# Optimization experiments

Hardware: AMD Instinct MI355X
Metric: run time of the kernel (lower is better)

## Reference

```python
import jax, jax.numpy as jnp
import numpy as np
from jax import lax

H = 8          # num_heads
STATE = 16     # SSM state_dim
EPS = 1e-5


def layer_norm(x, g, b):
    mu = jnp.mean(x, axis=-1, keepdims=True)
    var = jnp.mean((x - mu) ** 2, axis=-1, keepdims=True)
    return (x - mu) / jnp.sqrt(var + EPS) * g + b


def linear(x, w, b):
    # torch nn.Linear convention: w [out,in]
    return x @ w.T + b


def cross_attn(q_in, kv_in, qw, qb, kw, kb, vw, vb, ow, ob, g, beta):
    B, Lq, D = q_in.shape
    Lk = kv_in.shape[1]
    hd = D // H
    Q = linear(q_in, qw, qb).reshape(B, Lq, H, hd).transpose(0, 2, 1, 3)
    K = linear(kv_in, kw, kb).reshape(B, Lk, H, hd).transpose(0, 2, 1, 3)
    V = linear(kv_in, vw, vb).reshape(B, Lk, H, hd).transpose(0, 2, 1, 3)
    scores = jnp.einsum('bhqd,bhkd->bhqk', Q, K) / (hd ** 0.5)
    w = jax.nn.softmax(scores, axis=-1)
    out = jnp.einsum('bhqk,bhkd->bhqd', w, V)
    out = out.transpose(0, 2, 1, 3).reshape(B, Lq, D)
    out = linear(out, ow, ob)
    out = layer_norm(out + q_in, g, beta)
    return out, w


def ssm(x, in_w, in_b, A, Bm, C, gw, gb, ow, ob):
    B, L, D = x.shape
    xp = linear(x, in_w, in_b)                      # [B,L,2D]
    x_in = xp[..., D:]                              # second chunk
    gate = jax.nn.sigmoid(linear(x, gw, gb))
    x_in = x_in * gate
    def step(h, xt):
        h = h @ A.T + xt @ Bm.T                     # [B,STATE]
        return h, h @ C.T                           # y [B,D]
    h0 = jnp.zeros((B, STATE), dtype=x.dtype)
    _, ys = lax.scan(step, h0, x_in.transpose(1, 0, 2))
    ys = ys.transpose(1, 0, 2)
    return linear(ys, ow, ob)


def mamba_block(x, p, i):
    y = ssm(layer_norm(x, p['m_ln1_g'][i], p['m_ln1_b'][i]),
            p['m_in_w'][i], p['m_in_b'][i], p['m_A'][i], p['m_B'][i], p['m_C'][i],
            p['m_gate_w'][i], p['m_gate_b'][i], p['m_sout_w'][i], p['m_sout_b'][i])
    x = x + y
    h = layer_norm(x, p['m_ln2_g'][i], p['m_ln2_b'][i])
    h = linear(h, p['m_f1_w'][i], p['m_f1_b'][i])
    h = jax.nn.gelu(h, approximate=False)
    h = linear(h, p['m_f2_w'][i], p['m_f2_b'][i])
    return x + h


def setup_inputs() -> dict:
    key = jax.random.key(0)
    ks = iter(jax.random.split(key, 64))
    B, L, D, BD, VD = 1024, 32, 256, 128, 256
    nB = 6
    def rn(shape, s=0.02):
        return jax.random.normal(next(ks), shape, dtype=jnp.float32) * s
    inp = {
        'ble_features': jax.random.normal(next(ks), (B, L, BD), dtype=jnp.float32),
        'visual_features': jax.random.normal(next(ks), (B, L, VD), dtype=jnp.float32),
        # modality projections
        'bp_w': rn((D, BD)), 'bp_b': jnp.zeros(D), 'bp_emb': rn((D,)),
        'bp_g': jnp.ones(D), 'bp_beta': jnp.zeros(D),
        'vp_w': rn((D, VD)), 'vp_b': jnp.zeros(D), 'vp_emb': rn((D,)),
        'vp_g': jnp.ones(D), 'vp_beta': jnp.zeros(D),
        # two cross-attentions stacked on axis 0: [0]=ble->vis, [1]=vis->ble
        'a_qw': rn((2, D, D)), 'a_qb': jnp.zeros((2, D)),
        'a_kw': rn((2, D, D)), 'a_kb': jnp.zeros((2, D)),
        'a_vw': rn((2, D, D)), 'a_vb': jnp.zeros((2, D)),
        'a_ow': rn((2, D, D)), 'a_ob': jnp.zeros((2, D)),
        'a_g': jnp.ones((2, D)), 'a_beta': jnp.zeros((2, D)),
        # 6 mamba blocks stacked on axis 0
        'm_ln1_g': jnp.ones((nB, D)), 'm_ln1_b': jnp.zeros((nB, D)),
        'm_in_w': rn((nB, 2 * D, D)), 'm_in_b': jnp.zeros((nB, 2 * D)),
        'm_A': rn((nB, STATE, STATE)), 'm_B': rn((nB, STATE, D)), 'm_C': rn((nB, D, STATE)),
        'm_gate_w': rn((nB, D, D)), 'm_gate_b': jnp.zeros((nB, D)),
        'm_sout_w': rn((nB, D, D)), 'm_sout_b': jnp.zeros((nB, D)),
        'm_ln2_g': jnp.ones((nB, D)), 'm_ln2_b': jnp.zeros((nB, D)),
        'm_f1_w': rn((nB, 4 * D, D)), 'm_f1_b': jnp.zeros((nB, 4 * D)),
        'm_f2_w': rn((nB, D, 4 * D)), 'm_f2_b': jnp.zeros((nB, D)),
        # final projection
        'fin_g': jnp.ones(D), 'fin_beta': jnp.zeros(D),
        'fin_w': rn((D, D)), 'fin_b': jnp.zeros(D),
    }
    return inp


def reference(ble_features, visual_features,
              bp_w, bp_b, bp_emb, bp_g, bp_beta,
              vp_w, vp_b, vp_emb, vp_g, vp_beta,
              a_qw, a_qb, a_kw, a_kb, a_vw, a_vb, a_ow, a_ob, a_g, a_beta,
              m_ln1_g, m_ln1_b, m_in_w, m_in_b, m_A, m_B, m_C,
              m_gate_w, m_gate_b, m_sout_w, m_sout_b,
              m_ln2_g, m_ln2_b, m_f1_w, m_f1_b, m_f2_w, m_f2_b,
              fin_g, fin_beta, fin_w, fin_b):
    ble = layer_norm(linear(ble_features, bp_w, bp_b) + bp_emb, bp_g, bp_beta)
    vis = layer_norm(linear(visual_features, vp_w, vp_b) + vp_emb, vp_g, vp_beta)
    # seq_len == target_length -> align_sequences is identity
    ble_att, w_b2v = cross_attn(ble, vis, a_qw[0], a_qb[0], a_kw[0], a_kb[0],
                                a_vw[0], a_vb[0], a_ow[0], a_ob[0], a_g[0], a_beta[0])
    vis_att, w_v2b = cross_attn(vis, ble, a_qw[1], a_qb[1], a_kw[1], a_kb[1],
                                a_vw[1], a_vb[1], a_ow[1], a_ob[1], a_g[1], a_beta[1])
    fused = ble_att + vis_att
    p = dict(m_ln1_g=m_ln1_g, m_ln1_b=m_ln1_b, m_in_w=m_in_w, m_in_b=m_in_b,
             m_A=m_A, m_B=m_B, m_C=m_C, m_gate_w=m_gate_w, m_gate_b=m_gate_b,
             m_sout_w=m_sout_w, m_sout_b=m_sout_b, m_ln2_g=m_ln2_g, m_ln2_b=m_ln2_b,
             m_f1_w=m_f1_w, m_f1_b=m_f1_b, m_f2_w=m_f2_w, m_f2_b=m_f2_b)
    for i in range(m_A.shape[0]):
        fused = mamba_block(fused, p, i)
    g = jnp.mean(fused, axis=1)
    g = layer_norm(g, fin_g, fin_beta)
    g = jax.nn.gelu(linear(g, fin_w, fin_b), approximate=False)
    wb = jnp.mean(w_b2v, axis=(1, 2, 3))
    wv = jnp.mean(w_v2b, axis=(1, 2, 3))
    tot = wb + wv + 1e-6
    return (g, wb / tot, wv / tot)
```

## Files before the change

### kernel.cpp

```cpp
#include <hip/hip_runtime.h>
#include <hip/hip_bf16.h>
#include <math.h>

static constexpr int Bsz  = 1024;
static constexpr int Lseq = 32;
static constexpr int Dm   = 256;
static constexpr int NROW = Bsz * Lseq;

typedef __attribute__((ext_vector_type(8))) short bf16x8;
typedef __attribute__((ext_vector_type(4))) float f32x4;

__device__ __forceinline__ float sigm_f(float x) {
    return 1.0f / (1.0f + __expf(-x));
}
__device__ __forceinline__ float gelu_f(float x) {
    const float u = x * (0.7978845608028654f + 0.0356774081f * x * x);
    return x * sigm_f(2.0f * u);
}
__device__ __forceinline__ float b2f(ushort u) {
    union { float f; uint v; } t; t.v = ((uint)u) << 16; return t.f;
}
__device__ __forceinline__ ushort f2b(float f) {
    union { float f; uint v; } t; t.f = f;
    const uint lsb = (t.v >> 16) & 1u;
    t.v += 0x7fffu + lsb;
    return (ushort)(t.v >> 16);
}

#define GLDS(gp, lp) __builtin_amdgcn_global_load_lds( \
    (const __attribute__((address_space(1))) void*)(gp), \
    (__attribute__((address_space(3))) void*)(lp), 16, 0, 0)

template<int ACT, bool OUTBF, int OMAP, int DUAL>
__global__ __launch_bounds__(256)
void mgemm(const ushort* __restrict__ X, const ushort* __restrict__ W,
           const ushort* __restrict__ W2,
           const float* __restrict__ b1, const float* __restrict__ b2,
           float* __restrict__ Cf, ushort* __restrict__ Cb,
           ushort* __restrict__ Cb2, int K, int M)
{
    __shared__ ushort As[4096];
    __shared__ ushort Bs[4096];
    __shared__ ushort Bs2[DUAL ? 4096 : 8];
    __shared__ ushort Rx[DUAL ? 4096 : 8192];
    const int tid = threadIdx.x;
    const int w = tid >> 6, l = tid & 63;

    int f = blockIdx.y * gridDim.x + blockIdx.x;
    const int nwg = gridDim.x * gridDim.y;
    if ((nwg & 7) == 0) f = (f & 7) * (nwg >> 3) + (f >> 3);
    const int n0 = (f / gridDim.x) << 7;
    const int m0 = (f % gridDim.x) << 7;

    const int ric  = l >> 2;
    const int slot = l & 3;
    const int rL0 = (w << 4) + ric;
    const int rL1 = rL0 + 64;
    const int sw0 = slot ^ ((rL0 >> 1) & 3);
    const int sw1 = slot ^ ((rL1 >> 1) & 3);
    const ushort* gA0 = X + (size_t)(n0 + rL0) * K + (sw0 << 3);
    const ushort* gA1 = X + (size_t)(n0 + rL1) * K + (sw1 << 3);
    const ushort* gB0 = W + (size_t)(m0 + rL0) * K + (sw0 << 3);
    const ushort* gB1 = W + (size_t)(m0 + rL1) * K + (sw1 << 3);
    const ushort* gC0 = nullptr; const ushort* gC1 = nullptr;
    if constexpr (DUAL) {
        gC0 = W2 + (size_t)(m0 + rL0) * K + (sw0 << 3);
        gC1 = W2 + (size_t)(m0 + rL1) * K + (sw1 << 3);
    }
    ushort* lA0 = As + ((size_t)w << 9);
    ushort* lA1 = As + ((size_t)(w + 4) << 9);
    ushort* lB0 = Bs + ((size_t)w << 9);
    ushort* lB1 = Bs + ((size_t)(w + 4) << 9);
    ushort* lC0 = Bs2 + ((size_t)w << 9);
    ushort* lC1 = Bs2 + ((size_t)(w + 4) << 9);

    const int wr = (w >> 1) & 1, wc = w & 1;
    const int cl = l & 15, kg = l >> 4;
    int aoff[4], boff[4];
    #pragma unroll
    for (int m = 0; m < 4; ++m) {
        const int r = wr * 64 + m * 16 + cl;
        aoff[m] = r * 32 + ((kg ^ ((r >> 1) & 3)) << 3);
    }
    #pragma unroll
    for (int n = 0; n < 4; ++n) {
        const int r = wc * 64 + n * 16 + cl;
        boff[n] = r * 32 + ((kg ^ ((r >> 1) & 3)) << 3);
    }

    f32x4 acc[4][4];
    f32x4 acc2[DUAL ? 4 : 1][DUAL ? 4 : 1];
    #pragma unroll
    for (int m = 0; m < 4; ++m)
        #pragma unroll
        for (int n = 0; n < 4; ++n) {
            acc[m][n] = (f32x4){0.f, 0.f, 0.f, 0.f};
            if constexpr (DUAL) acc2[m][n] = (f32x4){0.f, 0.f, 0.f, 0.f};
        }

    for (int kc = 0; kc < K; kc += 32) {
        GLDS(gA0, lA0); GLDS(gA1, lA1);
        GLDS(gB0, lB0); GLDS(gB1, lB1);
        gA0 += 32; gA1 += 32; gB0 += 32; gB1 += 32;
        if constexpr (DUAL) {
            GLDS(gC0, lC0); GLDS(gC1, lC1);
            gC0 += 32; gC1 += 32;
        }
        __syncthreads();
        bf16x8 av[4], bv[4];
        #pragma unroll
        for (int m = 0; m < 4; ++m) av[m] = *(const bf16x8*)(As + aoff[m]);
        #pragma unroll
        for (int n = 0; n < 4; ++n) bv[n] = *(const bf16x8*)(Bs + boff[n]);
        #pragma unroll
        for (int m = 0; m < 4; ++m)
            #pragma unroll
            for (int n = 0; n < 4; ++n)
                acc[m][n] = __builtin_amdgcn_mfma_f32_16x16x32_bf16(
                    av[m], bv[n], acc[m][n], 0, 0, 0);
        if constexpr (DUAL) {
            bf16x8 cv[4];
            #pragma unroll
            for (int n = 0; n < 4; ++n) cv[n] = *(const bf16x8*)(Bs2 + boff[n]);
            #pragma unroll
            for (int m = 0; m < 4; ++m)
                #pragma unroll
                for (int n = 0; n < 4; ++n)
                    acc2[m][n] = __builtin_amdgcn_mfma_f32_16x16x32_bf16(
                        av[m], cv[n], acc2[m][n], 0, 0, 0);
        }
        __syncthreads();
    }

    const int colb = m0 + wc * 64 + cl;
    const int rowb = n0 + wr * 64 + (kg << 2);
    float biasA[4], biasB[4];
    #pragma unroll
    for (int n = 0; n < 4; ++n) {
        biasA[n] = (b1 != nullptr) ? b1[colb + n * 16] : 0.0f;
        if constexpr (DUAL) biasB[n] = b2[colb + n * 16];
    }

    if constexpr (OUTBF || DUAL != 0) {
        ushort* Rw;
        if constexpr (DUAL) Rw = (w == 0) ? As : (w == 1) ? Bs : (w == 2) ? Bs2 : Rx;
        else                Rw = (w == 0) ? As : (w == 1) ? Bs : Rx + ((w - 2) << 12);
        const int rr = l >> 3, rc8 = (l & 7) << 3;
        const int nout = (DUAL == 2) ? 2 : 1;
        for (int which = 0; which < nout; ++which) {
            #pragma unroll
            for (int m = 0; m < 4; ++m)
                #pragma unroll
                for (int j = 0; j < 4; ++j) {
                    const int lrow = m * 16 + (kg << 2) + j;
                    #pragma unroll
                    for (int n = 0; n < 4; ++n) {
                        float v;
                        if (which == 0) {
                            v = acc[m][n][j] + biasA[n];
                            if constexpr (DUAL == 1)
                                v = sigm_f(v) * (acc2[m][n][j] + biasB[n]);
                            else if (ACT == 1) v = sigm_f(v);
                            else if (ACT == 2) v = gelu_f(v);
                        } else {
                            v = acc2[m][n][j] + biasB[n];
                        }
                        const int lcol = (n << 4) + cl;
                        Rw[lrow * 64 + (lcol ^ (((lrow >> 1) & 7) << 3))] = f2b(v);
                    }
                }
            ushort* dst = (which == 0) ? Cb : Cb2;
            #pragma unroll
            for (int p = 0; p < 8; ++p) {
                const int lrow = (p << 3) + rr;
                const bf16x8 v8 = *(const bf16x8*)(
                    Rw + lrow * 64 + (rc8 ^ (((lrow >> 1) & 7) << 3)));
                const size_t grow = (size_t)(n0 + wr * 64 + lrow);
                const int gcol = m0 + wc * 64 + rc8;
                size_t idx;
                if (OMAP == 1) idx = grow * 1024 + ((size_t)(gcol >> 4) << 5) + (gcol & 15);
                else           idx = grow * (size_t)M + gcol;
                *(bf16x8*)(dst + idx) = v8;
            }
        }
    } else {
        #pragma unroll
        for (int m = 0; m < 4; ++m)
            #pragma unroll
            for (int j = 0; j < 4; ++j) {
                const size_t row = (size_t)(rowb + m * 16 + j);
                #pragma unroll
                for (int n = 0; n < 4; ++n) {
                    float v = acc[m][n][j] + biasA[n];
                    if (ACT == 1) v = sigm_f(v);
                    else if (ACT == 2) v = gelu_f(v);
                    Cf[row * (size_t)M + colb + n * 16] = v;
                }
            }
    }
}

template<bool ADD_E, bool ACC_F, bool WRV, int LNOUT, bool HASB2>
__global__ __launch_bounds__(256)
void growln_k(const ushort* __restrict__ X, const ushort* __restrict__ W,
              const float* __restrict__ b1, const float* __restrict__ b2,
              const float* __restrict__ E, const float* __restrict__ g,
              const float* __restrict__ bt, float* __restrict__ Fres,
              ushort* __restrict__ Yb, int K)
{
    __shared__ ushort As[32 * 32];
    __shared__ ushort Bs[256 * 32];
    __shared__ float sred[32][2];
    __shared__ float qred[32][2];
    const int tid = threadIdx.x;
    const int w = tid >> 6, l = tid & 63;
    const int n0 = blockIdx.x << 5;
    const int rowg = w >> 1, colg = w & 1;

    const int ric = l >> 2, slot = l & 3;
    const ushort* gB[4]; ushort* lB[4];
    #pragma unroll
    for (int c = 0; c < 4; ++c) {
        const int rB = ((w << 2) + c) * 16 + ric;
        gB[c] = W + (size_t)rB * K + ((slot ^ ((rB >> 1) & 3)) << 3);
        lB[c] = Bs + (((w << 2) + c) << 9);
    }
    const ushort* gA = nullptr; ushort* lA = nullptr;
    if (w < 2) {
        const int rA = (w << 4) + ric;
        gA = X + (size_t)(n0 + rA) * K + ((slot ^ ((rA >> 1) & 3)) << 3);
        lA = As + (w << 9);
    }

    const int cl = l & 15, kg = l >> 4;
    const int ar = rowg * 16 + cl;
    const int aoff = ar * 32 + ((kg ^ ((ar >> 1) & 3)) << 3);
    int boff[8];
    #pragma unroll
    for (int n = 0; n < 8; ++n) {
        const int br = colg * 128 + n * 16 + cl;
        boff[n] = br * 32 + ((kg ^ ((br >> 1) & 3)) << 3);
    }

    f32x4 acc[8];
    #pragma unroll
    for (int n = 0; n < 8; ++n) acc[n] = (f32x4){0.f, 0.f, 0.f, 0.f};

    for (int kc = 0; kc < K; kc += 32) {
        #pragma unroll
        for (int c = 0; c < 4; ++c) { GLDS(gB[c], lB[c]); gB[c] += 32; }
        if (w < 2) { GLDS(gA, lA); gA += 32; }
        __syncthreads();
        const bf16x8 av = *(const bf16x8*)(As + aoff);
        #pragma unroll
        for (int n = 0; n < 8; ++n) {
            const bf16x8 bv = *(const bf16x8*)(Bs + boff[n]);
            acc[n] = __builtin_amdgcn_mfma_f32_16x16x32_bf16(av, bv, acc[n], 0, 0, 0);
        }
        __syncthreads();
    }

    float bA[8];
    #pragma unroll
    for (int n = 0; n < 8; ++n) {
        const int col = colg * 128 + n * 16 + cl;
        float v = (b1 != nullptr) ? b1[col] : 0.0f;
        if (HASB2) v += b2[col];
        bA[n] = v;
    }
    float gg[8], bb[8];
    if (LNOUT > 0) {
        #pragma unroll
        for (int n = 0; n < 8; ++n) {
            const int col = colg * 128 + n * 16 + cl;
            gg[n] = g[col]; bb[n] = bt[col];
        }
    }

    #pragma unroll
    for (int j = 0; j < 4; ++j) {
        const int lrow = rowg * 16 + (kg << 2) + j;
        const size_t rb = (size_t)(n0 + lrow) << 8;
        float s = 0.0f;
        #pragma unroll
        for (int n = 0; n < 8; ++n) {
            const size_t idx = rb + colg * 128 + n * 16 + cl;
            float x = acc[n][j] + bA[n];
            if (ADD_E) x += E[idx];
            if (ACC_F) x += Fres[idx];
            acc[n][j] = x; s += x;
        }
        if (WRV) {
            #pragma unroll
            for (int n = 0; n < 8; ++n)
                Fres[rb + colg * 128 + n * 16 + cl] = acc[n][j];
        }
        if (LNOUT > 0) {
            #pragma unroll
            for (int o = 1; o < 16; o <<= 1) s += __shfl_xor(s, o);
            if (cl == 0) sred[lrow][colg] = s;
        }
    }
    if (LNOUT > 0) {
        __syncthreads();
        float mu[4];
        #pragma unroll
        for (int j = 0; j < 4; ++j) {
            const int lrow = rowg * 16 + (kg << 2) + j;
            mu[j] = (sred[lrow][0] + sred[lrow][1]) * (1.0f / 256.0f);
            float q = 0.0f;
            #pragma unroll
            for (int n = 0; n < 8; ++n) { const float d = acc[n][j] - mu[j]; q += d * d; }
            #pragma unroll
            for (int o = 1; o < 16; o <<= 1) q += __shfl_xor(q, o);
            if (cl == 0) qred[lrow][colg] = q;
        }
        __syncthreads();
        #pragma unroll
        for (int j = 0; j < 4; ++j) {
            const int lrow = rowg * 16 + (kg << 2) + j;
            const size_t rb = (size_t)(n0 + lrow) << 8;
            const float rstd = rsqrtf((qred[lrow][0] + qred[lrow][1]) * (1.0f / 256.0f) + 1e-5f);
            #pragma unroll
            for (int n = 0; n < 8; ++n) {
                const float y = (acc[n][j] - mu[j]) * rstd * gg[n] + bb[n];
                const size_t idx = rb + colg * 128 + n * 16 + cl;
                if (LNOUT & 1) Yb[idx] = f2b(y);
                if (LNOUT == 2 || LNOUT == 3) Fres[idx] = y;
                if (LNOUT == 4) Fres[idx] += y;
            }
        }
    }
}

__global__ __launch_bounds__(256)
void ln_k(const float* __restrict__ X, const float* __restrict__ g,
          const float* __restrict__ bt, ushort* __restrict__ Yb)
{
    const int lane = threadIdx.x & 63;
    const int row  = (blockIdx.x << 2) + (threadIdx.x >> 6);
    const size_t base = (size_t)row * Dm + (lane << 2);
    float4 v = *reinterpret_cast<const float4*>(&X[base]);
    float s = v.x + v.y + v.z + v.w;
    #pragma unroll
    for (int o = 1; o < 64; o <<= 1) s += __shfl_xor(s, o);
    const float mu = s * (1.0f / 256.0f);
    const float d0 = v.x - mu, d1 = v.y - mu, d2 = v.z - mu, d3 = v.w - mu;
    float q = d0*d0 + d1*d1 + d2*d2 + d3*d3;
    #pragma unroll
    for (int o = 1; o < 64; o <<= 1) q += __shfl_xor(q, o);
    const float rstd = rsqrtf(q * (1.0f / 256.0f) + 1e-5f);
    const int c = lane << 2;
    const float4 gg = *reinterpret_cast<const float4*>(&g[c]);
    const float4 bb = *reinterpret_cast<const float4*>(&bt[c]);
    ushort4 ub;
    ub.x = f2b(d0*rstd*gg.x + bb.x); ub.y = f2b(d1*rstd*gg.y + bb.y);
    ub.z = f2b(d2*rstd*gg.z + bb.z); ub.w = f2b(d3*rstd*gg.w + bb.w);
    *reinterpret_cast<ushort4*>(&Yb[base]) = ub;
}

__global__ __launch_bounds__(256)
void attn_k(const ushort* __restrict__ Q, const ushort* __restrict__ K,
            const ushort* __restrict__ V, ushort* __restrict__ O)
{
    __shared__ float Qs[32][33], Ks[32][33], Vs[32][33], Ss[32][33];
    const int bh = blockIdx.x;
    const int b = bh >> 3, h = bh & 7;
    const int tid = threadIdx.x;
    const int r  = tid >> 3;
    const int c4 = (tid & 7) << 2;
    const size_t base = ((size_t)b * Lseq + r) * Dm + h * 32 + c4;
    {
        const ushort4 q = *reinterpret_cast<const ushort4*>(&Q[base]);
        Qs[r][c4+0]=b2f(q.x); Qs[r][c4+1]=b2f(q.y); Qs[r][c4+2]=b2f(q.z); Qs[r][c4+3]=b2f(q.w);
        const ushort4 k = *reinterpret_cast<const ushort4*>(&K[base]);
        Ks[r][c4+0]=b2f(k.x); Ks[r][c4+1]=b2f(k.y); Ks[r][c4+2]=b2f(k.z); Ks[r][c4+3]=b2f(k.w);
        const ushort4 v = *reinterpret_cast<const ushort4*>(&V[base]);
        Vs[r][c4+0]=b2f(v.x); Vs[r][c4+1]=b2f(v.y); Vs[r][c4+2]=b2f(v.z); Vs[r][c4+3]=b2f(v.w);
    }
    __syncthreads();
    float sc[4] = {0.f, 0.f, 0.f, 0.f};
    #pragma unroll
    for (int d = 0; d < 32; ++d) {
        const float qv = Qs[r][d];
        #pragma unroll
        for (int j = 0; j < 4; ++j) sc[j] = fmaf(qv, Ks[c4+j][d], sc[j]);
    }
    #pragma unroll
    for (int j = 0; j < 4; ++j) sc[j] *= 0.17677669529663687f;
    float mx = fmaxf(fmaxf(sc[0], sc[1]), fmaxf(sc[2], sc[3]));
    #pragma unroll
    for (int o = 1; o < 8; o <<= 1) mx = fmaxf(mx, __shfl_xor(mx, o));
    float sum = 0.f;
    #pragma unroll
    for (int j = 0; j < 4; ++j) { sc[j] = __expf(sc[j] - mx); sum += sc[j]; }
    #pragma unroll
    for (int o = 1; o < 8; o <<= 1) sum += __shfl_xor(sum, o);
    const float inv = 1.0f / sum;
    #pragma unroll
    for (int j = 0; j < 4; ++j) Ss[r][c4+j] = sc[j] * inv;
    __syncthreads();
    float o4[4] = {0.f, 0.f, 0.f, 0.f};
    #pragma unroll
    for (int k = 0; k < 32; ++k) {
        const float wv = Ss[r][k];
        #pragma unroll
        for (int j = 0; j < 4; ++j) o4[j] = fmaf(wv, Vs[k][c4+j], o4[j]);
    }
    ushort4 ob; ob.x=f2b(o4[0]); ob.y=f2b(o4[1]); ob.z=f2b(o4[2]); ob.w=f2b(o4[3]);
    *reinterpret_cast<ushort4*>(&O[base]) = ob;
}

__global__ __launch_bounds__(256)
void xb_gemm(const ushort* __restrict__ X, const ushort* __restrict__ Bw,
             ushort* __restrict__ XB)
{
    __shared__ ushort As[128 * 32];
    __shared__ ushort Bsf[16 * 256];
    const int tid = threadIdx.x;
    const int w = tid >> 6, l = tid & 63;
    const int n0 = blockIdx.x << 7;
    #pragma unroll
    for (int rep = 0; rep < 2; ++rep) {
        const int u = (rep << 8) + tid;
        const int r = u >> 5;
        const int c8 = (u & 31) << 3;
        const int di = (r * 256 + c8) ^ ((r & 7) << 3);
        *(bf16x8*)(Bsf + di) = *(const bf16x8*)(Bw + r * 256 + c8);
    }
    const int ric = l >> 2, slot = l & 3;
    const int rL0 = (w << 4) + ric, rL1 = rL0 + 64;
    const int sw0 = slot ^ ((rL0 >> 1) & 3), sw1 = slot ^ ((rL1 >> 1) & 3);
    const ushort* gA0 = X + (size_t)(n0 + rL0) * 256 + (sw0 << 3);
    const ushort* gA1 = X + (size_t)(n0 + rL1) * 256 + (sw1 << 3);
    ushort* lA0 = As + (w << 9);
    ushort* lA1 = As + ((w + 4) << 9);
    const int cl = l & 15, kg = l >> 4;
    int aoff[2];
    #pragma unroll
    for (int m = 0; m < 2; ++m) {
        const int r = w * 32 + m * 16 + cl;
        aoff[m] = r * 32 + ((kg ^ ((r >> 1) & 3)) << 3);
    }
    f32x4 acc[2] = {(f32x4){0.f,0.f,0.f,0.f}, (f32x4){0.f,0.f,0.f,0.f}};
    for (int kc = 0; kc < 256; kc += 32) {
        GLDS(gA0, lA0); GLDS(gA1, lA1);
        gA0 += 32; gA1 += 32;
        __syncthreads();
        const bf16x8 av0 = *(const bf16x8*)(As + aoff[0]);
        const bf16x8 av1 = *(const bf16x8*)(As + aoff[1]);
        const int bidx = (cl * 256 + kc + (kg << 3)) ^ ((cl & 7) << 3);
        const bf16x8 bv = *(const bf16x8*)(Bsf + bidx);
        acc[0] = __builtin_amdgcn_mfma_f32_16x16x32_bf16(av0, bv, acc[0], 0, 0, 0);
        acc[1] = __builtin_amdgcn_mfma_f32_16x16x32_bf16(av1, bv, acc[1], 0, 0, 0);
        __syncthreads();
    }
    #pragma unroll
    for (int m = 0; m < 2; ++m)
        #pragma unroll
        for (int j = 0; j < 4; ++j) {
            const int row = n0 + w * 32 + m * 16 + (kg << 2) + j;
            XB[(size_t)row * 16 + cl] = f2b(acc[m][j]);
        }
}

__global__ __launch_bounds__(256)
void powT_k(const float* __restrict__ A_all, ushort* __restrict__ T_all)
{
    __shared__ float P[2][16][16];
    __shared__ float Asm[16][16];
    const int layer = blockIdx.x;
    const float* A = A_all + layer * 256;
    ushort* T = T_all + (size_t)layer * 262144;
    const int tid = threadIdx.x;
    const int i = tid >> 4, j = tid & 15;
    Asm[i][j] = A[tid];
    const bf16x8 z = {0,0,0,0,0,0,0,0};
    for (int u = tid; u < 32768; u += 256)
        *(bf16x8*)(T + (size_t)u * 8) = z;
    P[0][i][j] = (i == j) ? 1.0f : 0.0f;
    __syncthreads();
    for (int k = 0; k < 32; ++k) {
        const float pv = P[k & 1][i][j];
        const ushort pb = f2b(pv);
        for (int tau = 0; tau + k < 32; ++tau)
            T[(size_t)((tau + k) * 16 + i) * 512 + tau * 16 + j] = pb;
        float acc = 0.0f;
        #pragma unroll
        for (int l2 = 0; l2 < 16; ++l2) acc = fmaf(P[k & 1][i][l2], Asm[l2][j], acc);
        P[(k & 1) ^ 1][i][j] = acc;
        __syncthreads();
    }
}

__global__ __launch_bounds__(256)
void zeroH_k(ushort* __restrict__ Hp)
{
    const int i = blockIdx.x * 256 + threadIdx.x;
    const bf16x8 z = {0,0,0,0,0,0,0,0};
    *(bf16x8*)(Hp + (size_t)i * 8) = z;
}

__global__ __launch_bounds__(256)
void wsc_k(const float* __restrict__ sw, const float* __restrict__ Cc,
           ushort* __restrict__ Wp)
{
    const int i = blockIdx.x >> 4;
    const int m = ((blockIdx.x & 15) << 4) + (threadIdx.x >> 4);
    const int s = threadIdx.x & 15;
    const float* swr = sw + ((size_t)i << 16) + (m << 8);
    const float* cc  = Cc + ((size_t)i << 12) + s;
    float acc = 0.0f;
    #pragma unroll 8
    for (int d = 0; d < 256; ++d) acc = fmaf(swr[d], cc[d << 4], acc);
    ushort* o = Wp + ((size_t)i << 13) + (m << 5);
    o[s] = f2b(acc);
    o[s + 16] = 0;
}

__global__ __launch_bounds__(256)
void meanL_k(const float* __restrict__ X, float* __restrict__ G)
{
    const int idx = blockIdx.x * 256 + threadIdx.x;
    const int b = idx >> 8, d = idx & 255;
    const float* xp = X + (size_t)b * (Lseq * Dm) + d;
    float s = 0.0f;
    #pragma unroll
    for (int t = 0; t < Lseq; ++t) s += xp[t << 8];
    G[idx] = s * (1.0f / 32.0f);
}

__global__ __launch_bounds__(256)
void fillw_k(float* __restrict__ out)
{
    const int i = blockIdx.x * 256 + threadIdx.x;
    const float wm = 1.0f / 32.0f;
    out[i] = wm / (wm + wm + 1e-6f);
}

__global__ __launch_bounds__(256)
void cast_k(const float* __restrict__ src, ushort* __restrict__ dst, int n4)
{
    const int i = blockIdx.x * 256 + threadIdx.x;
    if (i < n4) {
        const float4 v = reinterpret_cast<const float4*>(src)[i];
        ushort4 o; o.x = f2b(v.x); o.y = f2b(v.y); o.z = f2b(v.z); o.w = f2b(v.w);
        reinterpret_cast<ushort4*>(dst)[i] = o;
    }
}

__global__ __launch_bounds__(256)
void cast_inw_k(const float* __restrict__ src, ushort* __restrict__ dst)
{
    const int i = blockIdx.x * 256 + threadIdx.x;
    const int blk = i >> 14, rem = i & 16383;
    const float4 v = reinterpret_cast<const float4*>(
        src + (size_t)blk * 131072 + 65536)[rem];
    ushort4 o; o.x = f2b(v.x); o.y = f2b(v.y); o.z = f2b(v.z); o.w = f2b(v.w);
    reinterpret_cast<ushort4*>(dst)[i] = o;
}

extern "C" void kernel_launch(void* const* d_in, const int* in_sizes, int n_in,
                              void* d_out, int out_size, void* d_ws, size_t ws_size,
                              hipStream_t stream)
{
    const float* ble_f   = (const float*)d_in[0];
    const float* vis_f   = (const float*)d_in[1];
    const float* bp_w    = (const float*)d_in[2];
    const float* bp_b    = (const float*)d_in[3];
    const float* bp_emb  = (const float*)d_in[4];
    const float* bp_g    = (const float*)d_in[5];
    const float* bp_beta = (const float*)d_in[6];
    const float* vp_w    = (const float*)d_in[7];
    const float* vp_b    = (const float*)d_in[8];
    const float* vp_emb  = (const float*)d_in[9];
    const float* vp_g    = (const float*)d_in[10];
    const float* vp_beta = (const float*)d_in[11];
    const float* a_qw    = (const float*)d_in[12];
    const float* a_qb    = (const float*)d_in[13];
    const float* a_kw    = (const float*)d_in[14];
    const float* a_kb    = (const float*)d_in[15];
    const float* a_vw    = (const float*)d_in[16];
    const float* a_vb    = (const float*)d_in[17];
    const float* a_ow    = (const float*)d_in[18];
    const float* a_ob    = (const float*)d_in[19];
    const float* a_g     = (const float*)d_in[20];
    const float* a_beta  = (const float*)d_in[21];
    const float* m_ln1_g = (const float*)d_in[22];
    const float* m_ln1_b = (const float*)d_in[23];
    const float* m_in_w  = (const float*)d_in[24];
    const float* m_in_b  = (const float*)d_in[25];
    const float* m_A     = (const float*)d_in[26];
    const float* m_B     = (const float*)d_in[27];
    const float* m_C     = (const float*)d_in[28];
    const float* m_gw    = (const float*)d_in[29];
    const float* m_gb    = (const float*)d_in[30];
    const float* m_sw    = (const float*)d_in[31];
    const float* m_sb    = (const float*)d_in[32];
    const float* m_ln2_g = (const float*)d_in[33];
    const float* m_ln2_b = (const float*)d_in[34];
    const float* m_f1w   = (const float*)d_in[35];
    const float* m_f1b   = (const float*)d_in[36];
    const float* m_f2w   = (const float*)d_in[37];
    const float* m_f2b   = (const float*)d_in[38];
    const float* fin_g   = (const float*)d_in[39];
    const float* fin_beta= (const float*)d_in[40];
    const float* fin_w   = (const float*)d_in[41];
    const float* fin_b   = (const float*)d_in[42];

    float* out = (float*)d_out;
    float* ws  = (float*)d_ws;
    const size_t NDf = (size_t)NROW * Dm;

    float* F_res = ws;
    float* F0 = ws + 1 * NDf;
    float* F1 = ws + 2 * NDf;
    float* F2 = ws + 3 * NDf;
    ushort* S0 = (ushort*)(ws + 4 * NDf);
    ushort* S1 = S0 + NDf;
    ushort* S2 = S1 + NDf;
    ushort* S3 = S2 + NDf;
    ushort* S4 = S3 + NDf;
    ushort* Wa = S4 + NDf;
    ushort* W_bp  = Wa;
    ushort* W_vp  = W_bp + 32768;
    ushort* W_q   = W_vp + 65536;
    ushort* W_k   = W_q + 131072;
    ushort* W_v   = W_k + 131072;
    ushort* W_o   = W_v + 131072;
    ushort* W_g   = W_o + 131072;
    ushort* W_in  = W_g + 393216;
    ushort* W_f1  = W_in + 393216;
    ushort* W_f2  = W_f1 + 1572864;
    ushort* W_fin = W_f2 + 1572864;
    ushort* W_sc  = W_fin + 65536;
    ushort* Hpad  = W_sc + 49152;
    ushort* B_ble = (ushort*)F2;
    ushort* B_vis = B_ble + (size_t)NROW * 128;
    ushort* T_all = (ushort*)F2;
    ushort* W_bm  = T_all + 1572864;
    ushort* XBuf  = W_bm + 24576;

    const dim3 blk(256);
    auto cgrid = [](int n4) { return dim3((n4 + 255) / 256); };

    cast_k<<<cgrid(1048576), blk, 0, stream>>>(ble_f, B_ble, 1048576);
    cast_k<<<cgrid(2097152), blk, 0, stream>>>(vis_f, B_vis, 2097152);
    cast_k<<<cgrid(8192),   blk, 0, stream>>>(bp_w, W_bp, 8192);
    cast_k<<<cgrid(16384),  blk, 0, stream>>>(vp_w, W_vp, 16384);
    cast_k<<<cgrid(32768),  blk, 0, stream>>>(a_qw, W_q, 32768);
    cast_k<<<cgrid(32768),  blk, 0, stream>>>(a_kw, W_k, 32768);
    cast_k<<<cgrid(32768),  blk, 0, stream>>>(a_vw, W_v, 32768);
    cast_k<<<cgrid(32768),  blk, 0, stream>>>(a_ow, W_o, 32768);
    cast_k<<<cgrid(98304),  blk, 0, stream>>>(m_gw, W_g, 98304);
    cast_k<<<cgrid(393216), blk, 0, stream>>>(m_f1w, W_f1, 393216);
    cast_k<<<cgrid(393216), blk, 0, stream>>>(m_f2w, W_f2, 393216);
    cast_k<<<cgrid(16384),  blk, 0, stream>>>(fin_w, W_fin, 16384);
    cast_inw_k<<<cgrid(98304), blk, 0, stream>>>(m_in_w, W_in);
    wsc_k<<<96, blk, 0, stream>>>(m_sw, m_C, W_sc);

    auto gg = [](int M, int N) { return dim3(M / 128, N / 128); };
    const dim3 gRow(NROW / 32);

    growln_k<false,false,false,3,true><<<gRow, blk, 0, stream>>>(
        B_ble, W_bp, bp_b, bp_emb, nullptr, bp_g, bp_beta, F0, S0, 128);
    growln_k<false,false,false,3,true><<<gRow, blk, 0, stream>>>(
        B_vis, W_vp, vp_b, vp_emb, nullptr, vp_g, vp_beta, F1, S1, 256);

    for (int a = 0; a < 2; ++a) {
        const ushort* qin_b = (a == 0) ? S0 : S1;
        const ushort* kin_b = (a == 0) ? S1 : S0;
        const float*  qin_f = (a == 0) ? F0 : F1;
        const size_t wo = (size_t)a * 65536;
        const size_t bo = (size_t)a * 256;
        mgemm<0,true,0,0><<<gg(256, NROW), blk, 0, stream>>>(
            qin_b, W_q + wo, nullptr, a_qb + bo, nullptr, nullptr, S4, nullptr, 256, 256);
        mgemm<0,true,0,2><<<gg(256, NROW), blk, 0, stream>>>(
            kin_b, W_k + wo, W_v + wo, a_kb + bo, a_vb + bo, nullptr, S2, S3, 256, 256);
        attn_k<<<Bsz * 8, blk, 0, stream>>>(S4, S2, S3, S4);
        if (a == 0)
            growln_k<true,false,false,2,false><<<gRow, blk, 0, stream>>>(
                S4, W_o + wo, a_ob + bo, nullptr, qin_f, a_g + bo, a_beta + bo, F_res, nullptr, 256);
        else
            growln_k<true,false,false,4,false><<<gRow, blk, 0, stream>>>(
                S4, W_o + wo, a_ob + bo, nullptr, qin_f, a_g + bo, a_beta + bo, F_res, nullptr, 256);
    }

    powT_k<<<6, blk, 0, stream>>>(m_A, T_all);
    cast_k<<<cgrid(6144), blk, 0, stream>>>(m_B, W_bm, 6144);
    zeroH_k<<<512, blk, 0, stream>>>(Hpad);

    ln_k<<<NROW/4, blk, 0, stream>>>(F_res, m_ln1_g, m_ln1_b, S0);

    for (int i = 0; i < 6; ++i) {
        mgemm<0,true,0,1><<<gg(256, NROW), blk, 0, stream>>>(
            S0, W_g + (size_t)i*65536, W_in + (size_t)i*65536,
            m_gb + i*256, m_in_b + (size_t)i*512 + 256, nullptr, S2, nullptr, 256, 256);
        xb_gemm<<<NROW/128, blk, 0, stream>>>(S2, W_bm + (size_t)i*4096, XBuf);
        mgemm<0,true,1,0><<<gg(512, 1024), blk, 0, stream>>>(
            XBuf, T_all + (size_t)i*262144, nullptr, nullptr, nullptr, nullptr, Hpad, nullptr, 512, 512);
        growln_k<false,true,true,1,false><<<gRow, blk, 0, stream>>>(
            Hpad, W_sc + (size_t)i*8192, m_sb + i*256, nullptr, nullptr,
            m_ln2_g + i*256, m_ln2_b + i*256, F_res, S0, 32);
        mgemm<2,true,0,0><<<gg(1024, NROW), blk, 0, stream>>>(
            S0, W_f1 + (size_t)i*262144, nullptr, m_f1b + i*1024, nullptr, nullptr, S1, nullptr, 256, 1024);
        if (i < 5)
            growln_k<false,true,true,1,false><<<gRow, blk, 0, stream>>>(
                S1, W_f2 + (size_t)i*262144, m_f2b + i*256, nullptr, nullptr,
                m_ln1_g + (i+1)*256, m_ln1_b + (i+1)*256, F_res, S0, 1024);
        else
            growln_k<false,true,true,0,false><<<gRow, blk, 0, stream>>>(
                S1, W_f2 + (size_t)i*262144, m_f2b + i*256, nullptr, nullptr,
                nullptr, nullptr, F_res, nullptr, 1024);
    }

    meanL_k<<<(Bsz * Dm) / 256, blk, 0, stream>>>(F_res, F0);
    ln_k<<<Bsz/4, blk, 0, stream>>>(F0, fin_g, fin_beta, S1);
    mgemm<2,false,0,0><<<gg(256, Bsz), blk, 0, stream>>>(
        S1, W_fin, nullptr, fin_b, nullptr, out, nullptr, nullptr, 256, 256);
    fillw_k<<<8, blk, 0, stream>>>(out + (size_t)Bsz * Dm);
}
```

Measured before the change: 1.293 ms.

## Double GEMM K-tile depth to 64 in mgemm and growln kernels

Raises the per-iteration K chunk from 32 to 64 in both the generic tiled GEMM and the row GEMM+layernorm kernel, halving the number of barrier-separated load/compute iterations. LDS tiles grow and use a new 8-way XOR swizzle. Because K must now be a multiple of 64, the padded state buffer (Hpad) and the folded SSM output weights are re-laid out with 64-wide padding, doubling the padded work for the K=32 SSM projection. Larger LDS use may lower occupancy.

```diff
diff --git a/kernel.cpp b/kernel.cpp
--- a/kernel.cpp
+++ b/kernel.cpp
@@ -31,6 +31,7 @@
     (const __attribute__((address_space(1))) void*)(gp), \
     (__attribute__((address_space(3))) void*)(lp), 16, 0, 0)
 
+
 template<int ACT, bool OUTBF, int OMAP, int DUAL>
 __global__ __launch_bounds__(256)
 void mgemm(const ushort* __restrict__ X, const ushort* __restrict__ W,
@@ -39,10 +40,9 @@
            float* __restrict__ Cf, ushort* __restrict__ Cb,
            ushort* __restrict__ Cb2, int K, int M)
 {
-    __shared__ ushort As[4096];
-    __shared__ ushort Bs[4096];
-    __shared__ ushort Bs2[DUAL ? 4096 : 8];
-    __shared__ ushort Rx[DUAL ? 4096 : 8192];
+    __shared__ ushort As[8192];
+    __shared__ ushort Bs[8192];
+    __shared__ ushort Bs2[DUAL ? 8192 : 8];
     const int tid = threadIdx.x;
     const int w = tid >> 6, l = tid & 63;
 
@@ -52,40 +52,40 @@
     const int n0 = (f / gridDim.x) << 7;
     const int m0 = (f % gridDim.x) << 7;
 
-    const int ric  = l >> 2;
-    const int slot = l & 3;
-    const int rL0 = (w << 4) + ric;
-    const int rL1 = rL0 + 64;
-    const int sw0 = slot ^ ((rL0 >> 1) & 3);
-    const int sw1 = slot ^ ((rL1 >> 1) & 3);
-    const ushort* gA0 = X + (size_t)(n0 + rL0) * K + (sw0 << 3);
-    const ushort* gA1 = X + (size_t)(n0 + rL1) * K + (sw1 << 3);
-    const ushort* gB0 = W + (size_t)(m0 + rL0) * K + (sw0 << 3);
-    const ushort* gB1 = W + (size_t)(m0 + rL1) * K + (sw1 << 3);
-    const ushort* gC0 = nullptr; const ushort* gC1 = nullptr;
-    if constexpr (DUAL) {
-        gC0 = W2 + (size_t)(m0 + rL0) * K + (sw0 << 3);
-        gC1 = W2 + (size_t)(m0 + rL1) * K + (sw1 << 3);
-    }
-    ushort* lA0 = As + ((size_t)w << 9);
-    ushort* lA1 = As + ((size_t)(w + 4) << 9);
-    ushort* lB0 = Bs + ((size_t)w << 9);
-    ushort* lB1 = Bs + ((size_t)(w + 4) << 9);
-    ushort* lC0 = Bs2 + ((size_t)w << 9);
-    ushort* lC1 = Bs2 + ((size_t)(w + 4) << 9);
+    const int ric = l >> 3;
+    const int sl  = l & 7;
+    const ushort* gAp[4]; const ushort* gBp[4]; const ushort* gCp[DUAL ? 4 : 1];
+    ushort* lAp[4]; ushort* lBp[4]; ushort* lCp[DUAL ? 4 : 1];
+    #pragma unroll
+    for (int c = 0; c < 4; ++c) {
+        const int r = ((w << 2) + c) * 8 + ric;
+        const int eo = (sl ^ (r & 7)) << 3;
+        gAp[c] = X + (size_t)(n0 + r) * K + eo;
+        gBp[c] = W + (size_t)(m0 + r) * K + eo;
+        lAp[c] = As + (((w << 2) + c) << 9) ;
+        lBp[c] = Bs + (((w << 2) + c) << 9);
+        if constexpr (DUAL) {
+            gCp[c] = W2 + (size_t)(m0 + r) * K + eo;
+            lCp[c] = Bs2 + (((w << 2) + c) << 9);
+        }
+    }
 
     const int wr = (w >> 1) & 1, wc = w & 1;
     const int cl = l & 15, kg = l >> 4;
-    int aoff[4], boff[4];
-    #pragma unroll
-    for (int m = 0; m < 4; ++m) {
-        const int r = wr * 64 + m * 16 + cl;
-        aoff[m] = r * 32 + ((kg ^ ((r >> 1) & 3)) << 3);
-    }
-    #pragma unroll
-    for (int n = 0; n < 4; ++n) {
-        const int r = wc * 64 + n * 16 + cl;
-        boff[n] = r * 32 + ((kg ^ ((r >> 1) & 3)) << 3);
+    int aoff[2][4], boff[2][4];
+    #pragma unroll
+    for (int sub = 0; sub < 2; ++sub) {
+        const int s = sub * 4 + kg;
+        #pragma unroll
+        for (int m = 0; m < 4; ++m) {
+            const int r = wr * 64 + m * 16 + cl;
+            aoff[sub][m] = r * 64 + ((s ^ (r & 7)) << 3);
+        }
+        #pragma unroll
+        for (int n = 0; n < 4; ++n) {
+            const int r = wc * 64 + n * 16 + cl;
+            boff[sub][n] = r * 64 + ((s ^ (r & 7)) << 3);
+        }
     }
 
     f32x4 acc[4][4];
@@ -98,36 +98,38 @@
             if constexpr (DUAL) acc2[m][n] = (f32x4){0.f, 0.f, 0.f, 0.f};
         }
 
-    for (int kc = 0; kc < K; kc += 32) {
-        GLDS(gA0, lA0); GLDS(gA1, lA1);
-        GLDS(gB0, lB0); GLDS(gB1, lB1);
-        gA0 += 32; gA1 += 32; gB0 += 32; gB1 += 32;
-        if constexpr (DUAL) {
-            GLDS(gC0, lC0); GLDS(gC1, lC1);
-            gC0 += 32; gC1 += 32;
-        }
-        __syncthreads();
-        bf16x8 av[4], bv[4];
-        #pragma unroll
-        for (int m = 0; m < 4; ++m) av[m] = *(const bf16x8*)(As + aoff[m]);
-        #pragma unroll
-        for (int n = 0; n < 4; ++n) bv[n] = *(const bf16x8*)(Bs + boff[n]);
-        #pragma unroll
-        for (int m = 0; m < 4; ++m)
-            #pragma unroll
-            for (int n = 0; n < 4; ++n)
-                acc[m][n] = __builtin_amdgcn_mfma_f32_16x16x32_bf16(
-                    av[m], bv[n], acc[m][n], 0, 0, 0);
-        if constexpr (DUAL) {
-            bf16x8 cv[4];
-            #pragma unroll
-            for (int n = 0; n < 4; ++n) cv[n] = *(const bf16x8*)(Bs2 + boff[n]);
+    for (int kc = 0; kc < K; kc += 64) {
+        #pragma unroll
+        for (int c = 0; c < 4; ++c) {
+            GLDS(gAp[c], lAp[c]); gAp[c] += 64;
+            GLDS(gBp[c], lBp[c]); gBp[c] += 64;
+            if constexpr (DUAL) { GLDS(gCp[c], lCp[c]); gCp[c] += 64; }
+        }
+        __syncthreads();
+        #pragma unroll
+        for (int sub = 0; sub < 2; ++sub) {
+            bf16x8 av[4], bv[4];
+            #pragma unroll
+            for (int m = 0; m < 4; ++m) av[m] = *(const bf16x8*)(As + aoff[sub][m]);
+            #pragma unroll
+            for (int n = 0; n < 4; ++n) bv[n] = *(const bf16x8*)(Bs + boff[sub][n]);
             #pragma unroll
             for (int m = 0; m < 4; ++m)
                 #pragma unroll
                 for (int n = 0; n < 4; ++n)
-                    acc2[m][n] = __builtin_amdgcn_mfma_f32_16x16x32_bf16(
-                        av[m], cv[n], acc2[m][n], 0, 0, 0);
+                    acc[m][n] = __builtin_amdgcn_mfma_f32_16x16x32_bf16(
+                        av[m], bv[n], acc[m][n], 0, 0, 0);
+            if constexpr (DUAL) {
+                bf16x8 cv[4];
+                #pragma unroll
+                for (int n = 0; n < 4; ++n) cv[n] = *(const bf16x8*)(Bs2 + boff[sub][n]);
+                #pragma unroll
+                for (int m = 0; m < 4; ++m)
+                    #pragma unroll
+                    for (int n = 0; n < 4; ++n)
+                        acc2[m][n] = __builtin_amdgcn_mfma_f32_16x16x32_bf16(
+                            av[m], cv[n], acc2[m][n], 0, 0, 0);
+            }
         }
         __syncthreads();
     }
@@ -142,9 +144,8 @@
     }
 
     if constexpr (OUTBF || DUAL != 0) {
-        ushort* Rw;
-        if constexpr (DUAL) Rw = (w == 0) ? As : (w == 1) ? Bs : (w == 2) ? Bs2 : Rx;
-        else                Rw = (w == 0) ? As : (w == 1) ? Bs : Rx + ((w - 2) << 12);
+        ushort* Rw = (w == 0) ? As : (w == 1) ? As + 4096
+                   : (w == 2) ? Bs : Bs + 4096;
         const int rr = l >> 3, rc8 = (l & 7) << 3;
         const int nout = (DUAL == 2) ? 2 : 1;
         for (int which = 0; which < nout; ++which) {
@@ -178,7 +179,7 @@
                 const size_t grow = (size_t)(n0 + wr * 64 + lrow);
                 const int gcol = m0 + wc * 64 + rc8;
                 size_t idx;
-                if (OMAP == 1) idx = grow * 1024 + ((size_t)(gcol >> 4) << 5) + (gcol & 15);
+                if (OMAP == 1) idx = grow * 2048 + ((size_t)(gcol >> 4) << 6) + (gcol & 15);
                 else           idx = grow * (size_t)M + gcol;
                 *(bf16x8*)(dst + idx) = v8;
             }
@@ -208,8 +209,8 @@
               const float* __restrict__ bt, float* __restrict__ Fres,
               ushort* __restrict__ Yb, int K)
 {
-    __shared__ ushort As[32 * 32];
-    __shared__ ushort Bs[256 * 32];
+    __shared__ ushort As[32 * 64];
+    __shared__ ushort Bs[256 * 64];
     __shared__ float sred[32][2];
     __shared__ float qred[32][2];
     const int tid = threadIdx.x;
@@ -217,45 +218,49 @@
     const int n0 = blockIdx.x << 5;
     const int rowg = w >> 1, colg = w & 1;
 
-    const int ric = l >> 2, slot = l & 3;
-    const ushort* gB[4]; ushort* lB[4];
-    #pragma unroll
-    for (int c = 0; c < 4; ++c) {
-        const int rB = ((w << 2) + c) * 16 + ric;
-        gB[c] = W + (size_t)rB * K + ((slot ^ ((rB >> 1) & 3)) << 3);
-        lB[c] = Bs + (((w << 2) + c) << 9);
-    }
-    const ushort* gA = nullptr; ushort* lA = nullptr;
-    if (w < 2) {
-        const int rA = (w << 4) + ric;
-        gA = X + (size_t)(n0 + rA) * K + ((slot ^ ((rA >> 1) & 3)) << 3);
-        lA = As + (w << 9);
-    }
+    const int ric = l >> 3, sl = l & 7;
+    const ushort* gB[8]; ushort* lB[8];
+    #pragma unroll
+    for (int c = 0; c < 8; ++c) {
+        const int rB = ((w << 3) + c) * 8 + ric;
+        gB[c] = W + (size_t)rB * K + ((sl ^ (rB & 7)) << 3);
+        lB[c] = Bs + (((w << 3) + c) << 9);
+    }
+    const int rA = (w << 3) + ric;
+    const ushort* gA = X + (size_t)(n0 + rA) * K + ((sl ^ (rA & 7)) << 3);
+    ushort* lA = As + (w << 9);
 
     const int cl = l & 15, kg = l >> 4;
     const int ar = rowg * 16 + cl;
-    const int aoff = ar * 32 + ((kg ^ ((ar >> 1) & 3)) << 3);
-    int boff[8];
-    #pragma unroll
-    for (int n = 0; n < 8; ++n) {
-        const int br = colg * 128 + n * 16 + cl;
-        boff[n] = br * 32 + ((kg ^ ((br >> 1) & 3)) << 3);
+    int aoff[2], boff[2][8];
+    #pragma unroll
+    for (int sub = 0; sub < 2; ++sub) {
+        const int s = sub * 4 + kg;
+        aoff[sub] = ar * 64 + ((s ^ (ar & 7)) << 3);
+        #pragma unroll
+        for (int n = 0; n < 8; ++n) {
+            const int br = colg * 128 + n * 16 + cl;
+            boff[sub][n] = br * 64 + ((s ^ (br & 7)) << 3);
+        }
     }
 
     f32x4 acc[8];
     #pragma unroll
     for (int n = 0; n < 8; ++n) acc[n] = (f32x4){0.f, 0.f, 0.f, 0.f};
 
-    for (int kc = 0; kc < K; kc += 32) {
-        #pragma unroll
-        for (int c = 0; c < 4; ++c) { GLDS(gB[c], lB[c]); gB[c] += 32; }
-        if (w < 2) { GLDS(gA, lA); gA += 32; }
-        __syncthreads();
-        const bf16x8 av = *(const bf16x8*)(As + aoff);
-        #pragma unroll
-        for (int n = 0; n < 8; ++n) {
-            const bf16x8 bv = *(const bf16x8*)(Bs + boff[n]);
-            acc[n] = __builtin_amdgcn_mfma_f32_16x16x32_bf16(av, bv, acc[n], 0, 0, 0);
+    for (int kc = 0; kc < K; kc += 64) {
+        #pragma unroll
+        for (int c = 0; c < 8; ++c) { GLDS(gB[c], lB[c]); gB[c] += 64; }
+        GLDS(gA, lA); gA += 64;
+        __syncthreads();
+        #pragma unroll
+        for (int sub = 0; sub < 2; ++sub) {
+            const bf16x8 av = *(const bf16x8*)(As + aoff[sub]);
+            #pragma unroll
+            for (int n = 0; n < 8; ++n) {
+                const bf16x8 bv = *(const bf16x8*)(Bs + boff[sub][n]);
+                acc[n] = __builtin_amdgcn_mfma_f32_16x16x32_bf16(av, bv, acc[n], 0, 0, 0);
+            }
         }
         __syncthreads();
     }
@@ -513,9 +518,9 @@
     float acc = 0.0f;
     #pragma unroll 8
     for (int d = 0; d < 256; ++d) acc = fmaf(swr[d], cc[d << 4], acc);
-    ushort* o = Wp + ((size_t)i << 13) + (m << 5);
+    ushort* o = Wp + ((size_t)i << 14) + (m << 6);
     o[s] = f2b(acc);
-    o[s + 16] = 0;
+    o[s + 16] = 0; o[s + 32] = 0; o[s + 48] = 0;
 }
 
 __global__ __launch_bounds__(256)
@@ -634,7 +639,7 @@
     ushort* W_f2  = W_f1 + 1572864;
     ushort* W_fin = W_f2 + 1572864;
     ushort* W_sc  = W_fin + 65536;
-    ushort* Hpad  = W_sc + 49152;
+    ushort* Hpad  = W_sc + 98304;
     ushort* B_ble = (ushort*)F2;
     ushort* B_vis = B_ble + (size_t)NROW * 128;
     ushort* T_all = (ushort*)F2;
@@ -688,7 +693,7 @@
 
     powT_k<<<6, blk, 0, stream>>>(m_A, T_all);
     cast_k<<<cgrid(6144), blk, 0, stream>>>(m_B, W_bm, 6144);
-    zeroH_k<<<512, blk, 0, stream>>>(Hpad);
+    zeroH_k<<<1024, blk, 0, stream>>>(Hpad);
 
     ln_k<<<NROW/4, blk, 0, stream>>>(F_res, m_ln1_g, m_ln1_b, S0);
 
@@ -700,8 +705,8 @@
         mgemm<0,true,1,0><<<gg(512, 1024), blk, 0, stream>>>(
             XBuf, T_all + (size_t)i*262144, nullptr, nullptr, nullptr, nullptr, Hpad, nullptr, 512, 512);
         growln_k<false,true,true,1,false><<<gRow, blk, 0, stream>>>(
-            Hpad, W_sc + (size_t)i*8192, m_sb + i*256, nullptr, nullptr,
-            m_ln2_g + i*256, m_ln2_b + i*256, F_res, S0, 32);
+            Hpad, W_sc + (size_t)i*16384, m_sb + i*256, nullptr, nullptr,
+            m_ln2_g + i*256, m_ln2_b + i*256, F_res, S0, 64);
         mgemm<2,true,0,0><<<gg(1024, NROW), blk, 0, stream>>>(
             S0, W_f1 + (size_t)i*262144, nullptr, m_f1b + i*1024, nullptr, nullptr, S1, nullptr, 256, 1024);
         if (i < 5)
```

New measurement: 1.165 ms. -9.9%, faster.
